# Optimization experiments

Hardware: AMD Instinct MI355X
Metric: run time of the kernel (lower is better)

Reference implementation:

```python
import jax, jax.numpy as jnp
from jax import lax
import numpy as np

DN = ('NCHW', 'OIHW', 'NCHW')

def conv2d(x, w, b, pad):
    y = lax.conv_general_dilated(x, w, (1, 1), [(pad, pad), (pad, pad)], dimension_numbers=DN)
    return y + b[None, :, None, None]

def setup_inputs() -> dict:
    key = jax.random.key(0)
    ks = jax.random.split(key, 20)
    B, C, H, W = 2, 256, 64, 64
    d = {}
    d['Fl'] = jax.random.normal(ks[0], (B, C, H, W), dtype=jnp.float32)
    d['Fv'] = jax.random.normal(ks[1], (B, C, H, W), dtype=jnp.float32)
    s3 = 1.0 / np.sqrt(C * 9)
    s1 = 1.0 / np.sqrt(C)
    names3 = ['Wqs', 'Wks', 'Wvs', 'Wqc', 'Wkc', 'Wvc']
    for i, n in enumerate(names3):
        d[n] = jax.random.normal(ks[2 + 2 * i], (C, C, 3, 3), dtype=jnp.float32) * s3
        d['b' + n[1:]] = jax.random.normal(ks[3 + 2 * i], (C,), dtype=jnp.float32) * 0.01
    d['Wgs'] = jax.random.normal(ks[14], (C, C, 1, 1), dtype=jnp.float32) * s1
    d['bgs'] = jax.random.normal(ks[15], (C,), dtype=jnp.float32) * 0.01
    d['Wfuse'] = jax.random.normal(ks[16], (C, 2 * C, 1, 1), dtype=jnp.float32) * (1.0 / np.sqrt(2 * C))
    d['bfuse'] = jax.random.normal(ks[17], (C,), dtype=jnp.float32) * 0.01
    return d

def reference(Fl, Fv, Wqs, bqs, Wks, bks, Wvs, bvs, Wqc, bqc, Wkc, bkc, Wvc, bvc, Wgs, bgs, Wfuse, bfuse):
    b, c, h, w = Fl.shape
    hw = h * w
    # --- self branch (on Fl) ---
    Qs = conv2d(Fl, Wqs, bqs, 1).reshape(b, c, hw)
    Ks = conv2d(Fl, Wks, bks, 1).reshape(b, c, hw)
    Vs = conv2d(Fl, Wvs, bvs, 1).reshape(b, c, hw)
    multi_s = jnp.einsum('bjk,bjq->bkq', Qs, Ks)          # [b, hw, hw]
    multi_s = jax.nn.softmax(multi_s, axis=1)              # softmax over dim=1 (as in torch code)
    Gs = jnp.einsum('bik,bjk->bij', multi_s, Vs)           # [b, hw, c]
    Gs = Gs.reshape(b, c, h, w)                            # raw reshape, faithful to torch
    Gs = conv2d(Gs, Wgs, bgs, 0) + Fl
    # --- cross branch (Q from Fl, K/V from Fv) ---
    Qc = conv2d(Fl, Wqc, bqc, 1).reshape(b, c, hw)
    Kc = conv2d(Fv, Wkc, bkc, 1).reshape(b, c, hw)
    Vc = conv2d(Fv, Wvc, bvc, 1).reshape(b, c, hw)
    multi_c = jnp.einsum('bjk,bjq->bkq', Qc, Kc)
    multi_c = jax.nn.softmax(multi_c, axis=1)
    Gc = jnp.einsum('bik,bjk->bij', multi_c, Vc)
    Gc = Gc.reshape(b, c, h, w)
    Gc = conv2d(Gc, Wgs, bgs, 0) + Fv                      # note: original uses Gs_conv for both branches
    out = conv2d(jnp.concatenate([Gs, Gc], axis=1), Wfuse, bfuse, 0)
    return out
```

## Files before the change

### kernel.cpp

```cpp
#include <hip/hip_runtime.h>

typedef __bf16 bf16x4 __attribute__((ext_vector_type(4)));
typedef __bf16 bf16x8 __attribute__((ext_vector_type(8)));
typedef float  f32x4  __attribute__((ext_vector_type(4)));

#define HWSZ 4096
#define CCH  256
#define LOG2E 1.44269504088896340736f

__device__ __forceinline__ float exp2_fast(float x) {
#if __has_builtin(__builtin_amdgcn_exp2f)
  return __builtin_amdgcn_exp2f(x);
#else
  return exp2f(x);
#endif
}

__device__ __forceinline__ void stage16(const __bf16* g, __bf16* ldsBase) {
#if __has_builtin(__builtin_amdgcn_global_load_lds)
  __builtin_amdgcn_global_load_lds(
      (const __attribute__((address_space(1))) void*)g,
      (__attribute__((address_space(3))) void*)ldsBase, 16, 0, 0);
#else
  int lane = threadIdx.x & 63;
  *(bf16x8*)(ldsBase + lane * 8) = *(const bf16x8*)g;
#endif
}

__global__ __launch_bounds__(256)
void gemm_conv(const __bf16* __restrict__ AL, const __bf16* __restrict__ AV,
               const __bf16* __restrict__ Cc,
               __bf16* __restrict__ qst, __bf16* __restrict__ kst,
               __bf16* __restrict__ vs,  __bf16* __restrict__ qct,
               __bf16* __restrict__ kct, __bf16* __restrict__ vc,
               const float* __restrict__ bqs, const float* __restrict__ bks,
               const float* __restrict__ bvs, const float* __restrict__ bqc,
               const float* __restrict__ bkc, const float* __restrict__ bvc)
{
  __shared__ __align__(16) __bf16 smem[8192];
  __bf16* As = smem;
  __bf16* Bs = smem + 4096;

  const int tid  = threadIdx.x;
  const int lane = tid & 63;
  const int w    = tid >> 6;
  const int wm   = (w >> 1) * 64;
  const int wn   = (w & 1) * 64;
  const int z    = blockIdx.z;
  const int by   = blockIdx.y;
  const int bn   = blockIdx.x * 128;
  const int K    = 2304;

  const bool isL = (by < 8);
  const int bm = (isL ? by : by - 8) * 128;
  const __bf16* Ab = isL ? AL : AV;
  const __bf16* Bb = Cc + (long)((isL ? 0 : 2) + z) * 9437184;

  f32x4 acc[4][4] = {};
  const int srow = lane >> 2;
  const int skc  = (lane & 3) * 8;

  for (int k0 = 0; k0 < K; k0 += 32) {
#pragma unroll
    for (int j = 0; j < 2; ++j) {
      int rbase = w * 32 + j * 16;
      stage16(Ab + (long)(bm + rbase + srow) * K + k0 + skc, As + rbase * 32);
    }
#pragma unroll
    for (int j = 0; j < 2; ++j) {
      int rbase = w * 32 + j * 16;
      stage16(Bb + (long)(bn + rbase + srow) * K + k0 + skc, Bs + rbase * 32);
    }
    __syncthreads();
    bf16x8 af[4], bfr[4];
#pragma unroll
    for (int t = 0; t < 4; ++t)
      af[t] = *(const bf16x8*)(As + (wm + t * 16 + (lane & 15)) * 32 + (lane >> 4) * 8);
#pragma unroll
    for (int t = 0; t < 4; ++t)
      bfr[t] = *(const bf16x8*)(Bs + (wn + t * 16 + (lane & 15)) * 32 + (lane >> 4) * 8);
#pragma unroll
    for (int mt = 0; mt < 4; ++mt)
#pragma unroll
      for (int nt = 0; nt < 4; ++nt)
        acc[mt][nt] = __builtin_amdgcn_mfma_f32_16x16x32_bf16(af[mt], bfr[nt], acc[mt][nt], 0, 0, 0);
    __syncthreads();
  }

#pragma unroll
  for (int mt = 0; mt < 4; ++mt) {
#pragma unroll
    for (int nt = 0; nt < 4; ++nt) {
#pragma unroll
      for (int r = 0; r < 4; ++r) {
        int m = bm + wm + mt * 16 + (lane >> 4) * 4 + r;
        int n = bn + wn + nt * 16 + (lane & 15);
        int g = m >> 8, mm = m & 255;
        const float* bias; __bf16* op; bool vlay;
        if (isL) {
          bias = (g == 0) ? bqs : (g == 1) ? bks : (g == 2) ? bvs : bqc;
          op   = (g == 0) ? qst : (g == 1) ? kst : (g == 2) ? vs  : qct;
          vlay = (g == 2);
        } else {
          bias = g ? bvc : bkc;
          op   = g ? vc  : kct;
          vlay = (g == 1);
        }
        float vv = acc[mt][nt][r] + bias[mm];
        if (vlay) op[(long)z * 1048576 + (long)mm * HWSZ + n] = (__bf16)vv;
        else      op[(long)z * 1048576 + (long)n * CCH + mm] = (__bf16)vv;
      }
    }
  }
}

__global__ __launch_bounds__(256)
void qk_stats(const __bf16* __restrict__ qs, const __bf16* __restrict__ qc,
              const __bf16* __restrict__ ks, const __bf16* __restrict__ kc,
              float* __restrict__ mst, float* __restrict__ lst)
{
  __shared__ __align__(16) __bf16 Kres[64 * 260];
  __shared__ float wm_[4][64], wl_[4][64];

  const int tid = threadIdx.x, lane = tid & 63, w = tid >> 6;
  const int quad = lane >> 4, l15 = lane & 15;
  const int lid = blockIdx.x;
  const int g = lid & 3;
  const int z = g & 1, br = g >> 1;
  const int qb = (lid >> 2) * 64;
  const __bf16* Qt = (br ? qc : qs) + (long)z * 1048576;
  const __bf16* Kt = (br ? kc : ks) + (long)z * 1048576;

  for (int idx = tid; idx < 2048; idx += 256) {
    int r = idx >> 5, c8 = (idx & 31) * 8;
    *(bf16x8*)(Kres + r * 260 + c8) = *(const bf16x8*)(Kt + (long)(qb + r) * 256 + c8);
  }
  __syncthreads();

  float rm[4], rl[4];
#pragma unroll
  for (int nt = 0; nt < 4; ++nt) { rm[nt] = -3.0e38f; rl[nt] = 0.f; }

  for (int it = 0; it < 16; ++it) {
    const int i0 = it * 256 + w * 64;
    f32x4 accS[4][4] = {};
#pragma unroll
    for (int cs = 0; cs < 256; cs += 32) {
      bf16x8 a[4], b[4];
#pragma unroll
      for (int mt = 0; mt < 4; ++mt)
        a[mt] = *(const bf16x8*)(Qt + (long)(i0 + mt * 16 + l15) * 256 + cs + quad * 8);
#pragma unroll
      for (int nt = 0; nt < 4; ++nt)
        b[nt] = *(const bf16x8*)(Kres + (nt * 16 + l15) * 260 + cs + quad * 8);
#pragma unroll
      for (int mt = 0; mt < 4; ++mt)
#pragma unroll
        for (int nt = 0; nt < 4; ++nt)
          accS[mt][nt] = __builtin_amdgcn_mfma_f32_16x16x32_bf16(a[mt], b[nt], accS[mt][nt], 0, 0, 0);
    }
#pragma unroll
    for (int nt = 0; nt < 4; ++nt) {
      float mx = -3.0e38f;
#pragma unroll
      for (int mt = 0; mt < 4; ++mt)
#pragma unroll
        for (int r = 0; r < 4; ++r) mx = fmaxf(mx, accS[mt][nt][r]);
      float sl = 0.f;
#pragma unroll
      for (int mt = 0; mt < 4; ++mt)
#pragma unroll
        for (int r = 0; r < 4; ++r) sl += exp2_fast((accS[mt][nt][r] - mx) * LOG2E);
#pragma unroll
      for (int d = 16; d <= 32; d <<= 1) {
        float om = __shfl_xor(mx, d, 64);
        float ol = __shfl_xor(sl, d, 64);
        float nm = fmaxf(mx, om);
        sl = sl * exp2_fast((mx - nm) * LOG2E) + ol * exp2_fast((om - nm) * LOG2E);
        mx = nm;
      }
      float nm = fmaxf(rm[nt], mx);
      rl[nt] = rl[nt] * exp2_fast((rm[nt] - nm) * LOG2E) + sl * exp2_fast((mx - nm) * LOG2E);
      rm[nt] = nm;
    }
  }
  if (lane < 16) {
#pragma unroll
    for (int nt = 0; nt < 4; ++nt) { wm_[w][nt * 16 + lane] = rm[nt]; wl_[w][nt * 16 + lane] = rl[nt]; }
  }
  __syncthreads();
  if (tid < 64) {
    float m = -3.0e38f;
#pragma unroll
    for (int ww = 0; ww < 4; ++ww) m = fmaxf(m, wm_[ww][tid]);
    float l = 0.f;
#pragma unroll
    for (int ww = 0; ww < 4; ++ww)
      l += wl_[ww][tid] * exp2_fast((wm_[ww][tid] - m) * LOG2E);
    long o = ((long)(br * 2 + z)) * 4096 + qb + tid;
    mst[o] = m;
    lst[o] = 1.0f / l;
  }
}

__global__ __launch_bounds__(256)
void fused_pv(const __bf16* __restrict__ qs, const __bf16* __restrict__ qc,
              const __bf16* __restrict__ ks, const __bf16* __restrict__ kc,
              const __bf16* __restrict__ vs, const __bf16* __restrict__ vc,
              const float* __restrict__ mst, const float* __restrict__ lst,
              float* __restrict__ gacc)
{
  __shared__ __align__(16) __bf16 Kst[2][128 * 32];
  __shared__ __align__(16) __bf16 Pl[64 * 132];

  const int tid = threadIdx.x, lane = tid & 63, w = tid >> 6;
  const int quad = lane >> 4, l15 = lane & 15;
  const int lid = blockIdx.x;
  const int g   = lid & 7;
  const int zbr = g >> 1;
  const int qh  = g & 1;
  const int bi  = (lid >> 3) * 64;
  const int br = zbr >> 1, z = zbr & 1;
  const __bf16* Qt = (br ? qc : qs) + (long)z * 1048576;
  const __bf16* Kt = (br ? kc : ks) + (long)z * 1048576;
  const __bf16* Vv = (br ? vc : vs) + (long)z * 1048576;
  const float* msp = mst + (long)zbr * 4096;
  const float* lsp = lst + (long)zbr * 4096;
  float* go = gacc + ((long)qh * 4 + zbr) * 1048576;

  bf16x8 aqr[8];
#pragma unroll
  for (int c8 = 0; c8 < 8; ++c8)
    aqr[c8] = *(const bf16x8*)(Qt + (long)(bi + w * 16 + l15) * 256 + c8 * 32 + quad * 8);

  f32x4 accO[4][4] = {};
  const int srow = lane >> 2, skc = (lane & 3) * 8;
  const int q0 = qh * 2048;

  for (int qt = 0; qt < 16; ++qt) {
    const int qc0 = q0 + qt * 128;
#pragma unroll
    for (int jj = 0; jj < 2; ++jj) {
      int rbase = w * 32 + jj * 16;
      stage16(Kt + (long)(qc0 + rbase + srow) * 256 + skc, Kst[0] + rbase * 32);
    }
    __syncthreads();
    f32x4 accS[8] = {};
#pragma unroll
    for (int cs = 0; cs < 8; ++cs) {
      if (cs < 7) {
#pragma unroll
        for (int jj = 0; jj < 2; ++jj) {
          int rbase = w * 32 + jj * 16;
          stage16(Kt + (long)(qc0 + rbase + srow) * 256 + (cs + 1) * 32 + skc,
                  Kst[(cs + 1) & 1] + rbase * 32);
        }
      }
      const __bf16* kb = Kst[cs & 1];
#pragma unroll
      for (int nt = 0; nt < 8; ++nt) {
        bf16x8 bk = *(const bf16x8*)(kb + (nt * 16 + l15) * 32 + quad * 8);
        accS[nt] = __builtin_amdgcn_mfma_f32_16x16x32_bf16(aqr[cs], bk, accS[nt], 0, 0, 0);
      }
      __syncthreads();
    }
#pragma unroll
    for (int nt = 0; nt < 8; ++nt) {
      int q = nt * 16 + l15;
      float mq = msp[qc0 + q], lq = lsp[qc0 + q];
#pragma unroll
      for (int r = 0; r < 4; ++r) {
        int i = w * 16 + quad * 4 + r;
        Pl[i * 132 + q] = (__bf16)(exp2_fast((accS[nt][r] - mq) * LOG2E) * lq);
      }
    }
    __syncthreads();
#pragma unroll
    for (int qs0 = 0; qs0 < 128; qs0 += 32) {
      bf16x8 ap[4], bv[4];
#pragma unroll
      for (int mt = 0; mt < 4; ++mt)
        ap[mt] = *(const bf16x8*)(Pl + (mt * 16 + l15) * 132 + qs0 + quad * 8);
#pragma unroll
      for (int nt = 0; nt < 4; ++nt)
        bv[nt] = *(const bf16x8*)(Vv + (long)(w * 64 + nt * 16 + l15) * 4096 + qc0 + qs0 + quad * 8);
#pragma unroll
      for (int mt = 0; mt < 4; ++mt)
#pragma unroll
        for (int nt = 0; nt < 4; ++nt)
          accO[mt][nt] = __builtin_amdgcn_mfma_f32_16x16x32_bf16(ap[mt], bv[nt], accO[mt][nt], 0, 0, 0);
    }
  }
#pragma unroll
  for (int mt = 0; mt < 4; ++mt)
#pragma unroll
    for (int nt = 0; nt < 4; ++nt)
#pragma unroll
      for (int r = 0; r < 4; ++r) {
        int i = mt * 16 + quad * 4 + r;
        int j = w * 64 + nt * 16 + l15;
        go[(long)(bi + i) * 256 + j] = accO[mt][nt][r];
      }
}

__global__ __launch_bounds__(256)
void gsum_reshape(const float* __restrict__ ga, __bf16* __restrict__ gt) {
  __shared__ __bf16 lds[64 * 260];
  const int t = threadIdx.x, lane = t & 63, w = t >> 6;
  const int zbr = blockIdx.z;
  const int v   = blockIdx.y;
  const int jg  = blockIdx.x;
  const float* g0 = ga + (long)zbr * 1048576;
  const float* g1 = g0 + 4194304;
  for (int ci0 = 0; ci0 < 256; ci0 += 4) {
    int ci = ci0 + w;
    long src = (long)(ci * 16 + v) * 256 + jg * 64 + lane;
    lds[lane * 260 + ci] = (__bf16)(g0[src] + g1[src]);
  }
  __syncthreads();
  __bf16* out = gt + (long)zbr * 1048576 + ((long)v * 256 + jg * 64) * 256;
#pragma unroll
  for (int pp = 0; pp < 8; ++pp) {
    int idx = pp * 256 + t;
    int row = idx >> 5, c8 = (idx & 31) * 8;
    *(bf16x8*)(out + (long)row * 256 + c8) = *(const bf16x8*)(lds + row * 260 + c8);
  }
}

__global__ __launch_bounds__(256)
void wcomb(const float* __restrict__ Wgs, const float* __restrict__ bgs,
           const float* __restrict__ Wfu, const float* __restrict__ bfu,
           __bf16* __restrict__ WT, float* __restrict__ biasT)
{
  const int co = blockIdx.x, t = threadIdx.x;
  const float* wrow = Wfu + (long)co * 512;
  float accs = 0.f, accc = 0.f;
  for (int c = 0; c < 256; ++c) {
    float gv = Wgs[(long)c * 256 + t];
    accs = fmaf(wrow[c], gv, accs);
    accc = fmaf(wrow[c + 256], gv, accc);
  }
  __bf16* o = WT + (long)co * 1024;
  o[t]       = (__bf16)accs;
  o[256 + t] = (__bf16)accc;
  o[512 + t] = (__bf16)wrow[t];
  o[768 + t] = (__bf16)wrow[256 + t];
  __shared__ float red[256];
  red[t] = (wrow[t] + wrow[t + 256]) * bgs[t];
  __syncthreads();
  for (int s = 128; s > 0; s >>= 1) {
    if (t < s) red[t] += red[t + s];
    __syncthreads();
  }
  if (t == 0) biasT[co] = bfu[co] + red[0];
}

__global__ __launch_bounds__(256)
void tail_gemm(const __bf16* __restrict__ WT, const __bf16* __restrict__ GTS,
               const __bf16* __restrict__ Xt, const float* __restrict__ biasT,
               float* __restrict__ out)
{
  __shared__ __align__(16) __bf16 smem[8192];
  __bf16* As = smem;
  __bf16* Bs = smem + 4096;

  const int tid  = threadIdx.x;
  const int lane = tid & 63;
  const int w    = tid >> 6;
  const int wm   = (w >> 1) * 64;
  const int wn   = (w & 1) * 64;
  const int z    = blockIdx.z;
  const int bm   = blockIdx.y * 128;
  const int bn   = blockIdx.x * 128;

  const __bf16* Bsel[4] = {
    GTS + (long)z * 1048576, GTS + (long)(2 + z) * 1048576,
    Xt  + (long)z * 1048576, Xt  + (long)(2 + z) * 1048576
  };

  f32x4 acc[4][4] = {};
  const int srow = lane >> 2;
  const int skc  = (lane & 3) * 8;

  for (int k0 = 0; k0 < 1024; k0 += 32) {
    const __bf16* Bb = Bsel[k0 >> 8];
    const int kk = k0 & 255;
#pragma unroll
    for (int j = 0; j < 2; ++j) {
      int rbase = w * 32 + j * 16;
      stage16(WT + (long)(bm + rbase + srow) * 1024 + k0 + skc, As + rbase * 32);
    }
#pragma unroll
    for (int j = 0; j < 2; ++j) {
      int rbase = w * 32 + j * 16;
      stage16(Bb + (long)(bn + rbase + srow) * 256 + kk + skc, Bs + rbase * 32);
    }
    __syncthreads();
    bf16x8 af[4], bfr[4];
#pragma unroll
    for (int t = 0; t < 4; ++t)
      af[t] = *(const bf16x8*)(As + (wm + t * 16 + (lane & 15)) * 32 + (lane >> 4) * 8);
#pragma unroll
    for (int t = 0; t < 4; ++t)
      bfr[t] = *(const bf16x8*)(Bs + (wn + t * 16 + (lane & 15)) * 32 + (lane >> 4) * 8);
#pragma unroll
    for (int mt = 0; mt < 4; ++mt)
#pragma unroll
      for (int nt = 0; nt < 4; ++nt)
        acc[mt][nt] = __builtin_amdgcn_mfma_f32_16x16x32_bf16(af[mt], bfr[nt], acc[mt][nt], 0, 0, 0);
    __syncthreads();
  }

#pragma unroll
  for (int mt = 0; mt < 4; ++mt)
#pragma unroll
    for (int nt = 0; nt < 4; ++nt)
#pragma unroll
      for (int r = 0; r < 4; ++r) {
        int m = bm + wm + mt * 16 + (lane >> 4) * 4 + r;
        int n = bn + wn + nt * 16 + (lane & 15);
        out[((long)z * 256 + m) * HWSZ + n] = acc[mt][nt][r] + biasT[m];
      }
}

__global__ void transpose_cvt(const float* __restrict__ F0, const float* __restrict__ F1,
                              __bf16* __restrict__ Xt) {
  __shared__ float tile[32][33];
  int img = blockIdx.z;
  const float* src = (img < 2 ? F0 : F1) + (long)(img & 1) * (CCH * HWSZ);
  __bf16* dst = Xt + (long)img * (HWSZ * CCH);
  int p0 = blockIdx.x * 32, c0 = blockIdx.y * 32;
  int tx = threadIdx.x, ty = threadIdx.y;
#pragma unroll
  for (int j = 0; j < 32; j += 8)
    tile[ty + j][tx] = src[(long)(c0 + ty + j) * HWSZ + p0 + tx];
  __syncthreads();
#pragma unroll
  for (int j = 0; j < 32; j += 8)
    dst[(long)(p0 + ty + j) * CCH + c0 + tx] = (__bf16)tile[tx][ty + j];
}

__global__ void im2col_k(const __bf16* __restrict__ Xt, __bf16* __restrict__ Cc) {
  int img = blockIdx.y;
  int e = blockIdx.x * 256 + threadIdx.x;
  int p = e / 288;
  int c8 = e - p * 288;
  int t = c8 >> 5;
  int ci0 = (c8 & 31) * 8;
  int dy = t / 3 - 1, dx = t - (t / 3) * 3 - 1;
  int y = p >> 6, x = p & 63;
  int yy = y + dy, xx = x + dx;
  const __bf16* src = Xt + (long)img * (HWSZ * CCH);
  __bf16* dst = Cc + (long)img * 9437184 + (long)p * 2304 + t * 256 + ci0;
  uint4 v = make_uint4(0u, 0u, 0u, 0u);
  if ((unsigned)yy < 64u && (unsigned)xx < 64u)
    v = *(const uint4*)(src + (long)(yy * 64 + xx) * CCH + ci0);
  *(uint4*)dst = v;
}

struct W6 { const float* w[6]; };
__global__ void repack_w3(W6 wp, __bf16* __restrict__ AL, __bf16* __restrict__ AV) {
  int zi = blockIdx.y;
  int e = blockIdx.x * 256 + threadIdx.x;
  int co = e / 2304;
  int rem = e - co * 2304;
  int t = rem >> 8, ci = rem & 255;
  float v = wp.w[zi][(long)co * 2304 + ci * 9 + t];
  __bf16* dst = (zi < 4) ? (AL + (long)zi * 256 * 2304) : (AV + (long)(zi - 4) * 256 * 2304);
  dst[(long)co * 2304 + rem] = (__bf16)v;
}

extern "C" void kernel_launch(void* const* d_in, const int* in_sizes, int n_in,
                              void* d_out, int out_size, void* d_ws, size_t ws_size,
                              hipStream_t stream) {
  const float* Fl  = (const float*)d_in[0];
  const float* Fv  = (const float*)d_in[1];
  const float* Wqs = (const float*)d_in[2];  const float* bqs = (const float*)d_in[3];
  const float* Wks = (const float*)d_in[4];  const float* bks = (const float*)d_in[5];
  const float* Wvs = (const float*)d_in[6];  const float* bvs = (const float*)d_in[7];
  const float* Wqc = (const float*)d_in[8];  const float* bqc = (const float*)d_in[9];
  const float* Wkc = (const float*)d_in[10]; const float* bkc = (const float*)d_in[11];
  const float* Wvc = (const float*)d_in[12]; const float* bvc = (const float*)d_in[13];
  const float* Wgs = (const float*)d_in[14]; const float* bgs = (const float*)d_in[15];
  const float* Wfu = (const float*)d_in[16]; const float* bfu = (const float*)d_in[17];

  char* ws = (char*)d_ws;
  size_t off = 0;
  auto take = [&](size_t bytes) -> void* {
    void* p = ws + off; off = (off + bytes + 255) & ~(size_t)255; return p;
  };
  __bf16* QST  = (__bf16*)take(4194304);
  __bf16* KST  = (__bf16*)take(4194304);
  __bf16* QCT  = (__bf16*)take(4194304);
  __bf16* KCT  = (__bf16*)take(4194304);
  __bf16* VS   = (__bf16*)take(4194304);
  __bf16* VC   = (__bf16*)take(4194304);
  __bf16* GTS  = (__bf16*)take(8388608);
  __bf16* AL   = (__bf16*)take(4718592);
  __bf16* AV   = (__bf16*)take(2359296);
  __bf16* WT   = (__bf16*)take(524288);
  float*  BT   = (float*)take(1024);
  float*  MST  = (float*)take(65536);
  float*  LST  = (float*)take(65536);
  __bf16* Xt   = (__bf16*)take(8388608);
  size_t ovl = off;
  __bf16* Cc = (__bf16*)take(75497472);
  size_t needConv = off;
  float* GACC = (float*)(ws + ovl);
  size_t needAttn = ovl + 33554432;
  size_t need = needConv > needAttn ? needConv : needAttn;
  if (ws_size < need) return;

  transpose_cvt<<<dim3(128, 8, 4), dim3(32, 8), 0, stream>>>(Fl, Fv, Xt);
  im2col_k<<<dim3(4608, 4), 256, 0, stream>>>(Xt, Cc);
  W6 wp; wp.w[0]=Wqs; wp.w[1]=Wks; wp.w[2]=Wvs; wp.w[3]=Wqc; wp.w[4]=Wkc; wp.w[5]=Wvc;
  repack_w3<<<dim3(2304, 6), 256, 0, stream>>>(wp, AL, AV);
  wcomb<<<dim3(256), 256, 0, stream>>>(Wgs, bgs, Wfu, bfu, WT, BT);

  gemm_conv<<<dim3(32, 12, 2), 256, 0, stream>>>(
      AL, AV, Cc, QST, KST, VS, QCT, KCT, VC,
      bqs, bks, bvs, bqc, bkc, bvc);

  qk_stats<<<dim3(256), 256, 0, stream>>>(QST, QCT, KST, KCT, MST, LST);

  fused_pv<<<dim3(512), 256, 0, stream>>>(
      QST, QCT, KST, KCT, VS, VC, MST, LST, GACC);

  gsum_reshape<<<dim3(4, 16, 4), 256, 0, stream>>>(GACC, GTS);

  tail_gemm<<<dim3(32, 2, 2), 256, 0, stream>>>(WT, GTS, Xt, BT, (float*)d_out);
}
```

Baseline: 467.1 us.

## Split attention stats and PV reductions across more blocks for occupancy

The qk_stats kernel now splits the reduction dimension in half, doubling its block count to 512, and writes partial max/sum values. A new small combine kernel merges those partials into the final statistics. fused_pv is split four ways instead of two (1024 blocks), and gsum_reshape now sums four partial accumulators. The aim is better occupancy on the many-CU GPU, at the cost of an extra launch, twice the fp32 partial-output traffic and a larger workspace.

```diff
diff --git a/kernel.cpp b/kernel.cpp
--- a/kernel.cpp
+++ b/kernel.cpp
@@ -117,7 +117,7 @@
 __global__ __launch_bounds__(256)
 void qk_stats(const __bf16* __restrict__ qs, const __bf16* __restrict__ qc,
               const __bf16* __restrict__ ks, const __bf16* __restrict__ kc,
-              float* __restrict__ mst, float* __restrict__ lst)
+              float* __restrict__ pm, float* __restrict__ pl)
 {
   __shared__ __align__(16) __bf16 Kres[64 * 260];
   __shared__ float wm_[4][64], wl_[4][64];
@@ -127,7 +127,8 @@
   const int lid = blockIdx.x;
   const int g = lid & 3;
   const int z = g & 1, br = g >> 1;
-  const int qb = (lid >> 2) * 64;
+  const int ih = (lid >> 2) & 1;
+  const int qb = (lid >> 3) * 64;
   const __bf16* Qt = (br ? qc : qs) + (long)z * 1048576;
   const __bf16* Kt = (br ? kc : ks) + (long)z * 1048576;
 
@@ -141,8 +142,8 @@
 #pragma unroll
   for (int nt = 0; nt < 4; ++nt) { rm[nt] = -3.0e38f; rl[nt] = 0.f; }
 
-  for (int it = 0; it < 16; ++it) {
-    const int i0 = it * 256 + w * 64;
+  for (int it = 0; it < 8; ++it) {
+    const int i0 = ih * 2048 + it * 256 + w * 64;
     f32x4 accS[4][4] = {};
 #pragma unroll
     for (int cs = 0; cs < 256; cs += 32) {
@@ -197,10 +198,22 @@
 #pragma unroll
     for (int ww = 0; ww < 4; ++ww)
       l += wl_[ww][tid] * exp2_fast((wm_[ww][tid] - m) * LOG2E);
-    long o = ((long)(br * 2 + z)) * 4096 + qb + tid;
-    mst[o] = m;
-    lst[o] = 1.0f / l;
-  }
+    long o = ((long)ih * 4 + br * 2 + z) * 4096 + qb + tid;
+    pm[o] = m;
+    pl[o] = l;
+  }
+}
+
+__global__ void stats_combine2(const float* __restrict__ pm, const float* __restrict__ pl,
+                               float* __restrict__ mst, float* __restrict__ lst) {
+  int q = blockIdx.x * 256 + threadIdx.x;
+  int zbr = blockIdx.y;
+  float m0 = pm[(long)zbr * 4096 + q],        l0 = pl[(long)zbr * 4096 + q];
+  float m1 = pm[(long)(4 + zbr) * 4096 + q],  l1 = pl[(long)(4 + zbr) * 4096 + q];
+  float m = fmaxf(m0, m1);
+  float l = l0 * exp2_fast((m0 - m) * LOG2E) + l1 * exp2_fast((m1 - m) * LOG2E);
+  mst[(long)zbr * 4096 + q] = m;
+  lst[(long)zbr * 4096 + q] = 1.0f / l;
 }
 
 __global__ __launch_bounds__(256)
@@ -216,17 +229,17 @@
   const int tid = threadIdx.x, lane = tid & 63, w = tid >> 6;
   const int quad = lane >> 4, l15 = lane & 15;
   const int lid = blockIdx.x;
-  const int g   = lid & 7;
-  const int zbr = g >> 1;
-  const int qh  = g & 1;
-  const int bi  = (lid >> 3) * 64;
+  const int g   = lid & 15;
+  const int zbr = g >> 2;
+  const int qq  = g & 3;
+  const int bi  = (lid >> 4) * 64;
   const int br = zbr >> 1, z = zbr & 1;
   const __bf16* Qt = (br ? qc : qs) + (long)z * 1048576;
   const __bf16* Kt = (br ? kc : ks) + (long)z * 1048576;
   const __bf16* Vv = (br ? vc : vs) + (long)z * 1048576;
   const float* msp = mst + (long)zbr * 4096;
   const float* lsp = lst + (long)zbr * 4096;
-  float* go = gacc + ((long)qh * 4 + zbr) * 1048576;
+  float* go = gacc + ((long)qq * 4 + zbr) * 1048576;
 
   bf16x8 aqr[8];
 #pragma unroll
@@ -235,9 +248,9 @@
 
   f32x4 accO[4][4] = {};
   const int srow = lane >> 2, skc = (lane & 3) * 8;
-  const int q0 = qh * 2048;
-
-  for (int qt = 0; qt < 16; ++qt) {
+  const int q0 = qq * 1024;
+
+  for (int qt = 0; qt < 8; ++qt) {
     const int qc0 = q0 + qt * 128;
 #pragma unroll
     for (int jj = 0; jj < 2; ++jj) {
@@ -311,11 +324,11 @@
   const int v   = blockIdx.y;
   const int jg  = blockIdx.x;
   const float* g0 = ga + (long)zbr * 1048576;
-  const float* g1 = g0 + 4194304;
   for (int ci0 = 0; ci0 < 256; ci0 += 4) {
     int ci = ci0 + w;
     long src = (long)(ci * 16 + v) * 256 + jg * 64 + lane;
-    lds[lane * 260 + ci] = (__bf16)(g0[src] + g1[src]);
+    float s = g0[src] + g0[src + 4194304] + g0[src + 8388608] + g0[src + 12582912];
+    lds[lane * 260 + ci] = (__bf16)s;
   }
   __syncthreads();
   __bf16* out = gt + (long)zbr * 1048576 + ((long)v * 256 + jg * 64) * 256;
@@ -502,12 +515,14 @@
   float*  BT   = (float*)take(1024);
   float*  MST  = (float*)take(65536);
   float*  LST  = (float*)take(65536);
+  float*  PM   = (float*)take(131072);
+  float*  PL   = (float*)take(131072);
   __bf16* Xt   = (__bf16*)take(8388608);
   size_t ovl = off;
   __bf16* Cc = (__bf16*)take(75497472);
   size_t needConv = off;
   float* GACC = (float*)(ws + ovl);
-  size_t needAttn = ovl + 33554432;
+  size_t needAttn = ovl + 67108864;
   size_t need = needConv > needAttn ? needConv : needAttn;
   if (ws_size < need) return;
 
@@ -521,9 +536,10 @@
       AL, AV, Cc, QST, KST, VS, QCT, KCT, VC,
       bqs, bks, bvs, bqc, bkc, bvc);
 
-  qk_stats<<<dim3(256), 256, 0, stream>>>(QST, QCT, KST, KCT, MST, LST);
-
-  fused_pv<<<dim3(512), 256, 0, stream>>>(
+  qk_stats<<<dim3(512), 256, 0, stream>>>(QST, QCT, KST, KCT, PM, PL);
+  stats_combine2<<<dim3(16, 4), 256, 0, stream>>>(PM, PL, MST, LST);
+
+  fused_pv<<<dim3(1024), 256, 0, stream>>>(
       QST, QCT, KST, KCT, VS, VC, MST, LST, GACC);
 
   gsum_reshape<<<dim3(4, 16, 4), 256, 0, stream>>>(GACC, GTS);
```

New measurement: 456.2 us. 1.02x faster.
